# Optimization experiments

Hardware: AMD Instinct MI355X
Metric: run time of the kernel (lower is better)

## Reference

```python
import jax, jax.numpy as jnp
import numpy as np

# Model constants (match init_kwargs / torchcde conventions)
B = 1024        # batch
L = 128         # number of spline knots (grid_points = 0..L-1)
C_IN = 8        # input_channels
HID = 64        # hidden_channels
MLP_H = 128     # CDEFunc hidden width
INIT_H = 20     # initial-network hidden width


def setup_inputs() -> dict:
    key = jax.random.key(0)
    ks = jax.random.split(key, 9)
    # cubic spline coeffs: (B, L-1, 4*C_IN) laid out as [a, b, c, d] per interval
    coeffs = jax.random.normal(ks[0], (B, L - 1, 4 * C_IN), dtype=jnp.float32) * 0.1
    # initial network: C_IN -> 20 -> HID (ReLU, then Tanh)
    Wi1 = jax.random.normal(ks[1], (C_IN, INIT_H), dtype=jnp.float32) / np.sqrt(C_IN)
    bi1 = jnp.zeros((INIT_H,), jnp.float32)
    Wi2 = jax.random.normal(ks[2], (INIT_H, HID), dtype=jnp.float32) / np.sqrt(INIT_H)
    bi2 = jnp.zeros((HID,), jnp.float32)
    # CDE vector field: (HID+1) -> 128 -> C_IN*HID (ReLU, then Tanh)
    W1 = jax.random.normal(ks[3], (HID + 1, MLP_H), dtype=jnp.float32) / np.sqrt(HID + 1)
    b1 = jnp.zeros((MLP_H,), jnp.float32)
    W2 = jax.random.normal(ks[4], (MLP_H, C_IN * HID), dtype=jnp.float32) / np.sqrt(MLP_H)
    b2 = jnp.zeros((C_IN * HID,), jnp.float32)
    return {"coeffs": coeffs, "Wi1": Wi1, "bi1": bi1, "Wi2": Wi2, "bi2": bi2,
            "W1": W1, "b1": b1, "W2": W2, "b2": b2}


def reference(coeffs, Wi1, bi1, Wi2, bi2, W1, b1, W2, b2):
    Lm1 = coeffs.shape[1]
    # a,b,c,d: each (B, L-1, C_IN). X(t) = a + b*f + c*f^2 + d*f^3 on interval idx,
    # dX/dt = b + 2c*f + 3d*f^2, with f = t - idx (torchcde CubicSpline convention).
    a, b, c, d = jnp.split(coeffs, 4, axis=-1)

    def dXdt(t):
        idx = jnp.clip(jnp.floor(t).astype(jnp.int32), 0, Lm1 - 1)
        fr = t - idx
        return b[:, idx] + 2.0 * c[:, idx] * fr + 3.0 * d[:, idx] * fr * fr  # (B, C_IN)

    def cde_func(t, z):
        # FFN([HID+1, 128, C_IN*HID], ReLU hidden, Tanh output) on concat(t, z)
        tz = jnp.concatenate([jnp.full((z.shape[0], 1), t, z.dtype), z], axis=1)
        h = jax.nn.relu(tz @ W1 + b1)
        return jnp.tanh(h @ W2 + b2).reshape(z.shape[0], HID, C_IN)  # (B, HID, C_IN)

    def vf(t, z):
        # dz/dt = f(t,z) @ dX/dt
        return jnp.einsum('bhc,bc->bh', cde_func(t, z), dXdt(t))

    # z0 = initial(X(t0)); X(0) = a at interval 0 with frac 0
    X0 = a[:, 0]
    z0 = jnp.tanh(jax.nn.relu(X0 @ Wi1 + bi1) @ Wi2 + bi2)  # (B, HID)

    def rk4_step(z, i):
        t = i.astype(z.dtype)
        k1 = vf(t, z)
        k2 = vf(t + 0.5, z + 0.5 * k1)
        k3 = vf(t + 0.5, z + 0.5 * k2)
        k4 = vf(t + 1.0, z + k3)
        z_new = z + (k1 + 2.0 * k2 + 2.0 * k3 + k4) / 6.0
        return z_new, z_new

    _, zs = jax.lax.scan(rk4_step, z0, jnp.arange(Lm1))  # (L-1, B, HID)
    # z evaluated at all grid points, like cdeint(t=X.grid_points): (B, L, HID)
    return jnp.concatenate([z0[None], zs], axis=0).transpose(1, 0, 2)
```

## Files before the change

### kernel.cpp

```cpp
#include <hip/hip_runtime.h>
#include <stdint.h>

#define LM1  127
#define NTHR 512

typedef _Float16 half8_t __attribute__((ext_vector_type(8)));
typedef float    f32x4   __attribute__((ext_vector_type(4)));

__device__ __forceinline__ float fast_tanh(float x) {
  float e = __expf(2.0f * x);
  return 1.0f - 2.0f * __builtin_amdgcn_rcpf(e + 1.0f);
}

__global__ void __launch_bounds__(NTHR, 2) cde_kernel(
    const float* __restrict__ coeffs,
    const float* __restrict__ Wi1, const float* __restrict__ bi1,
    const float* __restrict__ Wi2, const float* __restrict__ bi2,
    const float* __restrict__ W1,  const float* __restrict__ b1,
    const float* __restrict__ W2,  const float* __restrict__ b2,
    float* __restrict__ out)
{
  __shared__ _Float16 zsb[16 * 72];
  __shared__ _Float16 hA [16 * 136];
  __shared__ float    fwb[8][284];
  __shared__ float    gds[2][3][4][8];

  const int t    = threadIdx.x;
  const int lane = t & 63;
  const int w    = t >> 6;
  const int l15  = lane & 15;
  const int lq   = lane >> 4;
  const int r    = lane & 3;
  const int hxl  = (lane >> 2) & 7;
  const int hx   = w * 8 + hxl;
  const int row0 = blockIdx.x * 4;
  const bool owner = (lane < 32);

  for (int u = t; u < 16 * 72 / 2;  u += NTHR) ((uint32_t*)zsb)[u] = 0u;
  for (int u = t; u < 16 * 136 / 2; u += NTHR) ((uint32_t*)hA)[u]  = 0u;

  half8_t bB[2];
  #pragma unroll
  for (int kt = 0; kt < 2; ++kt)
    #pragma unroll
    for (int j = 0; j < 8; ++j)
      bB[kt][j] = (_Float16)W1[(1 + kt * 32 + lq * 8 + j) * 128 + w * 16 + l15];
  const float w1t_c = W1[w * 16 + l15];
  const float b1_c  = b1[w * 16 + l15];

  half8_t bf[4][4];
  #pragma unroll
  for (int nt = 0; nt < 4; ++nt)
    #pragma unroll
    for (int kt = 0; kt < 4; ++kt)
      #pragma unroll
      for (int j = 0; j < 8; ++j)
        bf[nt][kt][j] =
            (_Float16)W2[(kt * 32 + lq * 8 + j) * 512 + w * 64 + nt * 16 + l15];

  float b2r[8];
  #pragma unroll
  for (int c = 0; c < 8; ++c) b2r[c] = b2[hx * 8 + c];

  float z = 0.0f;
  if (owner) {
    const float* cb = coeffs + (size_t)(row0 + r) * (LM1 * 32);
    float x0[8];
    #pragma unroll
    for (int c = 0; c < 8; ++c) x0[c] = cb[c];
    float acc = bi2[hx];
    for (int j = 0; j < 20; ++j) {
      float u = bi1[j];
      #pragma unroll
      for (int c = 0; c < 8; ++c) u += x0[c] * Wi1[c * 20 + j];
      acc += fmaxf(u, 0.0f) * Wi2[j * 64 + hx];
    }
    z = fast_tanh(acc);
    out[(size_t)(row0 + r) * 8192 + hx] = z;
  }

  const int rg = (t >> 3) & 3, cg = t & 7;
  const float* cbp = coeffs + (size_t)(row0 + rg) * (LM1 * 32);
  float pb = 0.f, pc = 0.f, pd = 0.f, pbn = 0.f;
  if (t < 32) { pb = cbp[8 + cg]; pc = cbp[16 + cg]; pd = cbp[24 + cg]; pbn = cbp[40 + cg]; }

  for (int i = 0; i < LM1; ++i) {
    if (t < 32) {
      gds[i & 1][0][rg][cg] = pb;
      gds[i & 1][1][rg][cg] = pb + pc + 0.75f * pd;
      gds[i & 1][2][rg][cg] = (i < LM1 - 1) ? pbn : fmaf(3.0f, pd, fmaf(2.0f, pc, pb));
      if (i + 1 < LM1) {
        const float* nb = cbp + (size_t)(i + 1) * 32;
        pb = nb[8 + cg]; pc = nb[16 + cg]; pd = nb[24 + cg];
        pbn = (i + 2 < LM1) ? nb[40 + cg] : 0.0f;
      }
    }

    float ksum = 0.0f, kprev = 0.0f;
    #pragma unroll
    for (int s = 0; s < 4; ++s) {
      const float coef = (s == 0) ? 0.0f : (s == 3) ? 1.0f : 0.5f;
      const float ts   = (float)i + ((s == 0) ? 0.0f : (s == 3) ? 1.0f : 0.5f);
      const int   gi   = (s == 0) ? 0 : (s == 3) ? 2 : 1;

      if (owner) zsb[r * 72 + hx] = (_Float16)(z + coef * kprev);
      __syncthreads();

      {
        half8_t a0 = *(const half8_t*)(zsb + l15 * 72 + lq * 8);
        half8_t a1 = *(const half8_t*)(zsb + l15 * 72 + 32 + lq * 8);
        f32x4 hd = {0.f, 0.f, 0.f, 0.f};
        hd = __builtin_amdgcn_mfma_f32_16x16x32_f16(a0, bB[0], hd, 0, 0, 0);
        hd = __builtin_amdgcn_mfma_f32_16x16x32_f16(a1, bB[1], hd, 0, 0, 0);
        if (lane < 16) {
          const float hb = fmaf(ts, w1t_c, b1_c);
          const int col = w * 16 + lane;
          hA[0 * 136 + col] = (_Float16)fmaxf(hd.x + hb, 0.0f);
          hA[1 * 136 + col] = (_Float16)fmaxf(hd.y + hb, 0.0f);
          hA[2 * 136 + col] = (_Float16)fmaxf(hd.z + hb, 0.0f);
          hA[3 * 136 + col] = (_Float16)fmaxf(hd.w + hb, 0.0f);
        }
      }
      __syncthreads();

      {
        half8_t ha[4];
        #pragma unroll
        for (int kt = 0; kt < 4; ++kt)
          ha[kt] = *(const half8_t*)(hA + l15 * 136 + kt * 32 + lq * 8);
        f32x4 d0 = {0.f,0.f,0.f,0.f}, d1 = d0, d2 = d0, d3 = d0;
        #pragma unroll
        for (int kt = 0; kt < 4; ++kt) {
          d0 = __builtin_amdgcn_mfma_f32_16x16x32_f16(ha[kt], bf[0][kt], d0, 0, 0, 0);
          d1 = __builtin_amdgcn_mfma_f32_16x16x32_f16(ha[kt], bf[1][kt], d1, 0, 0, 0);
          d2 = __builtin_amdgcn_mfma_f32_16x16x32_f16(ha[kt], bf[2][kt], d2, 0, 0, 0);
          d3 = __builtin_amdgcn_mfma_f32_16x16x32_f16(ha[kt], bf[3][kt], d3, 0, 0, 0);
        }
        if (lane < 16) {
          f32x4 dd[4] = {d0, d1, d2, d3};
          #pragma unroll
          for (int nt = 0; nt < 4; ++nt) {
            const int cl = nt * 16 + lane;
            *(f32x4*)(&fwb[w][36 * (cl >> 3) + 4 * (cl & 7)]) = dd[nt];
          }
        }
      }
      asm volatile("s_waitcnt lgkmcnt(0)" ::: "memory");

      if (owner) {
        const f32x4 g0 = *(const f32x4*)&gds[i & 1][gi][r][0];
        const f32x4 g1 = *(const f32x4*)&gds[i & 1][gi][r][4];
        const float gg[8] = {g0.x, g0.y, g0.z, g0.w, g1.x, g1.y, g1.z, g1.w};
        const float* fp = &fwb[w][36 * hxl + r];
        float kcv = 0.0f;
        #pragma unroll
        for (int c = 0; c < 8; ++c)
          kcv += fast_tanh(fp[4 * c] + b2r[c]) * gg[c];
        kprev = kcv;
        ksum += ((s == 1 || s == 2) ? 2.0f : 1.0f) * kcv;
      }
    }
    if (owner) {
      z += ksum * (1.0f / 6.0f);
      out[(size_t)(row0 + r) * 8192 + (size_t)(i + 1) * 64 + hx] = z;
    }
  }
}

extern "C" void kernel_launch(void* const* d_in, const int* in_sizes, int n_in,
                              void* d_out, int out_size, void* d_ws, size_t ws_size,
                              hipStream_t stream) {
  const float* coeffs = (const float*)d_in[0];
  const float* Wi1    = (const float*)d_in[1];
  const float* bi1    = (const float*)d_in[2];
  const float* Wi2    = (const float*)d_in[3];
  const float* bi2    = (const float*)d_in[4];
  const float* W1     = (const float*)d_in[5];
  const float* b1     = (const float*)d_in[6];
  const float* W2     = (const float*)d_in[7];
  const float* b2     = (const float*)d_in[8];
  float* out          = (float*)d_out;
  (void)in_sizes; (void)n_in; (void)out_size; (void)d_ws; (void)ws_size;
  cde_kernel<<<256, NTHR, 0, stream>>>(coeffs, Wi1, bi1, Wi2, bi2,
                                       W1, b1, W2, b2, out);
}
```

Measured before the change: 595.0 us.

## Split CDE vector-field work across 16 waves with swizzled LDS layouts

Doubles the block to 1024 threads so each wave computes half as many W2 output tiles (2 MFMA accumulators instead of 4). The tanh/dot epilogue is spread across all 64 lanes, with each lane handling 2 channels and combining results through xor shuffles. The z and hidden activations are stored in LDS in MFMA operand order so they can be read contiguously. The aim is to shorten the serial per-stage critical path of the RK4 loop, at the cost of more barrier participants and idle waves in the first GEMM.

```diff
diff --git a/kernel.cpp b/kernel.cpp
--- a/kernel.cpp
+++ b/kernel.cpp
@@ -2,17 +2,18 @@
 #include <stdint.h>
 
 #define LM1  127
-#define NTHR 512
+#define NTHR 1024
 
 typedef _Float16 half8_t __attribute__((ext_vector_type(8)));
 typedef float    f32x4   __attribute__((ext_vector_type(4)));
+typedef float    f32x2   __attribute__((ext_vector_type(2)));
 
 __device__ __forceinline__ float fast_tanh(float x) {
   float e = __expf(2.0f * x);
   return 1.0f - 2.0f * __builtin_amdgcn_rcpf(e + 1.0f);
 }
 
-__global__ void __launch_bounds__(NTHR, 2) cde_kernel(
+__global__ void __launch_bounds__(NTHR, 4) cde_kernel(
     const float* __restrict__ coeffs,
     const float* __restrict__ Wi1, const float* __restrict__ bi1,
     const float* __restrict__ Wi2, const float* __restrict__ bi2,
@@ -20,9 +21,9 @@
     const float* __restrict__ W2,  const float* __restrict__ b2,
     float* __restrict__ out)
 {
-  __shared__ _Float16 zsb[16 * 72];
-  __shared__ _Float16 hA [16 * 136];
-  __shared__ float    fwb[8][284];
+  __shared__ _Float16 zsb[1024];
+  __shared__ _Float16 hA [2048];
+  __shared__ float    fwb[16][144];
   __shared__ float    gds[2][3][4][8];
 
   const int t    = threadIdx.x;
@@ -31,39 +32,56 @@
   const int l15  = lane & 15;
   const int lq   = lane >> 4;
   const int r    = lane & 3;
-  const int hxl  = (lane >> 2) & 7;
-  const int hx   = w * 8 + hxl;
   const int row0 = blockIdx.x * 4;
-  const bool owner = (lane < 32);
 
-  for (int u = t; u < 16 * 72 / 2;  u += NTHR) ((uint32_t*)zsb)[u] = 0u;
-  for (int u = t; u < 16 * 136 / 2; u += NTHR) ((uint32_t*)hA)[u]  = 0u;
+  for (int u = t; u < 512;  u += NTHR) ((uint32_t*)zsb)[u] = 0u;
+  for (int u = t; u < 1024; u += NTHR) ((uint32_t*)hA)[u]  = 0u;
 
-  half8_t bB[2];
+  half8_t bB[2] = {};
+  float w1t_c = 0.f, b1_c = 0.f;
+  if (w < 8) {
+    #pragma unroll
+    for (int kt = 0; kt < 2; ++kt)
+      #pragma unroll
+      for (int j = 0; j < 8; ++j)
+        bB[kt][j] = (_Float16)W1[(1 + kt * 32 + lq * 8 + j) * 128 + w * 16 + l15];
+    w1t_c = W1[w * 16 + l15];
+    b1_c  = b1[w * 16 + l15];
+  }
+
+  half8_t bf[2][4];
   #pragma unroll
-  for (int kt = 0; kt < 2; ++kt)
-    #pragma unroll
-    for (int j = 0; j < 8; ++j)
-      bB[kt][j] = (_Float16)W1[(1 + kt * 32 + lq * 8 + j) * 128 + w * 16 + l15];
-  const float w1t_c = W1[w * 16 + l15];
-  const float b1_c  = b1[w * 16 + l15];
-
-  half8_t bf[4][4];
-  #pragma unroll
-  for (int nt = 0; nt < 4; ++nt)
+  for (int nt = 0; nt < 2; ++nt)
     #pragma unroll
     for (int kt = 0; kt < 4; ++kt)
       #pragma unroll
       for (int j = 0; j < 8; ++j)
         bf[nt][kt][j] =
-            (_Float16)W2[(kt * 32 + lq * 8 + j) * 512 + w * 64 + nt * 16 + l15];
+            (_Float16)W2[(kt * 32 + lq * 8 + j) * 512 + w * 32 + nt * 16 + l15];
 
-  float b2r[8];
-  #pragma unroll
-  for (int c = 0; c < 8; ++c) b2r[c] = b2[hx * 8 + c];
+  const int q    = lane >> 4;
+  const int hxlk = (lane >> 2) & 3;
+  const int hxk  = w * 4 + hxlk;
+  const float b2r0 = b2[hxk * 8 + 2 * q];
+  const float b2r1 = b2[hxk * 8 + 2 * q + 1];
+
+  const int hx = w * 4 + (lane >> 2);
+  _Float16* zwp;
+  {
+    const int kh = hx >> 5, lqw = (hx >> 3) & 3, j = hx & 7;
+    zwp = &zsb[8 * (kh * 64 + lqw * 16 + r) + j];
+  }
+  _Float16* hwp;
+  {
+    const int col = 16 * w + l15;
+    const int ktw = (col >> 5) & 3, lqw2 = (col >> 3) & 3, j2 = col & 7;
+    hwp = &hA[8 * (ktw * 64 + lqw2 * 16) + j2];
+  }
+  float* const fsp = &fwb[w][36 * (l15 >> 3) + 4 * (l15 & 7)];
+  const float* const frp = &fwb[w][36 * hxlk + 8 * q + r];
 
   float z = 0.0f;
-  if (owner) {
+  if (lane < 16) {
     const float* cb = coeffs + (size_t)(row0 + r) * (LM1 * 32);
     float x0[8];
     #pragma unroll
@@ -84,6 +102,8 @@
   float pb = 0.f, pc = 0.f, pd = 0.f, pbn = 0.f;
   if (t < 32) { pb = cbp[8 + cg]; pc = cbp[16 + cg]; pd = cbp[24 + cg]; pbn = cbp[40 + cg]; }
 
+  __syncthreads();
+
   for (int i = 0; i < LM1; ++i) {
     if (t < 32) {
       gds[i & 1][0][rg][cg] = pb;
@@ -103,22 +123,21 @@
       const float ts   = (float)i + ((s == 0) ? 0.0f : (s == 3) ? 1.0f : 0.5f);
       const int   gi   = (s == 0) ? 0 : (s == 3) ? 2 : 1;
 
-      if (owner) zsb[r * 72 + hx] = (_Float16)(z + coef * kprev);
+      if (lane < 16) *zwp = (_Float16)(z + coef * kprev);
       __syncthreads();
 
-      {
-        half8_t a0 = *(const half8_t*)(zsb + l15 * 72 + lq * 8);
-        half8_t a1 = *(const half8_t*)(zsb + l15 * 72 + 32 + lq * 8);
+      if (w < 8) {
+        const half8_t a0 = *(const half8_t*)(zsb + 8 * lane);
+        const half8_t a1 = *(const half8_t*)(zsb + 512 + 8 * lane);
         f32x4 hd = {0.f, 0.f, 0.f, 0.f};
         hd = __builtin_amdgcn_mfma_f32_16x16x32_f16(a0, bB[0], hd, 0, 0, 0);
         hd = __builtin_amdgcn_mfma_f32_16x16x32_f16(a1, bB[1], hd, 0, 0, 0);
         if (lane < 16) {
           const float hb = fmaf(ts, w1t_c, b1_c);
-          const int col = w * 16 + lane;
-          hA[0 * 136 + col] = (_Float16)fmaxf(hd.x + hb, 0.0f);
-          hA[1 * 136 + col] = (_Float16)fmaxf(hd.y + hb, 0.0f);
-          hA[2 * 136 + col] = (_Float16)fmaxf(hd.z + hb, 0.0f);
-          hA[3 * 136 + col] = (_Float16)fmaxf(hd.w + hb, 0.0f);
+          hwp[0]  = (_Float16)fmaxf(hd.x + hb, 0.0f);
+          hwp[8]  = (_Float16)fmaxf(hd.y + hb, 0.0f);
+          hwp[16] = (_Float16)fmaxf(hd.z + hb, 0.0f);
+          hwp[24] = (_Float16)fmaxf(hd.w + hb, 0.0f);
         }
       }
       __syncthreads();
@@ -127,40 +146,31 @@
         half8_t ha[4];
         #pragma unroll
         for (int kt = 0; kt < 4; ++kt)
-          ha[kt] = *(const half8_t*)(hA + l15 * 136 + kt * 32 + lq * 8);
-        f32x4 d0 = {0.f,0.f,0.f,0.f}, d1 = d0, d2 = d0, d3 = d0;
+          ha[kt] = *(const half8_t*)(hA + 512 * kt + 8 * lane);
+        f32x4 d0 = {0.f, 0.f, 0.f, 0.f}, d1 = d0;
         #pragma unroll
         for (int kt = 0; kt < 4; ++kt) {
           d0 = __builtin_amdgcn_mfma_f32_16x16x32_f16(ha[kt], bf[0][kt], d0, 0, 0, 0);
           d1 = __builtin_amdgcn_mfma_f32_16x16x32_f16(ha[kt], bf[1][kt], d1, 0, 0, 0);
-          d2 = __builtin_amdgcn_mfma_f32_16x16x32_f16(ha[kt], bf[2][kt], d2, 0, 0, 0);
-          d3 = __builtin_amdgcn_mfma_f32_16x16x32_f16(ha[kt], bf[3][kt], d3, 0, 0, 0);
         }
         if (lane < 16) {
-          f32x4 dd[4] = {d0, d1, d2, d3};
-          #pragma unroll
-          for (int nt = 0; nt < 4; ++nt) {
-            const int cl = nt * 16 + lane;
-            *(f32x4*)(&fwb[w][36 * (cl >> 3) + 4 * (cl & 7)]) = dd[nt];
-          }
+          *(f32x4*)(fsp)      = d0;
+          *(f32x4*)(fsp + 72) = d1;
         }
       }
       asm volatile("s_waitcnt lgkmcnt(0)" ::: "memory");
 
-      if (owner) {
-        const f32x4 g0 = *(const f32x4*)&gds[i & 1][gi][r][0];
-        const f32x4 g1 = *(const f32x4*)&gds[i & 1][gi][r][4];
-        const float gg[8] = {g0.x, g0.y, g0.z, g0.w, g1.x, g1.y, g1.z, g1.w};
-        const float* fp = &fwb[w][36 * hxl + r];
-        float kcv = 0.0f;
-        #pragma unroll
-        for (int c = 0; c < 8; ++c)
-          kcv += fast_tanh(fp[4 * c] + b2r[c]) * gg[c];
+      {
+        const float v0 = frp[0], v1 = frp[4];
+        const f32x2 gv = *(const f32x2*)&gds[i & 1][gi][r][2 * q];
+        float kcv = fast_tanh(v0 + b2r0) * gv.x + fast_tanh(v1 + b2r1) * gv.y;
+        kcv += __shfl_xor(kcv, 16, 64);
+        kcv += __shfl_xor(kcv, 32, 64);
         kprev = kcv;
         ksum += ((s == 1 || s == 2) ? 2.0f : 1.0f) * kcv;
       }
     }
-    if (owner) {
+    if (lane < 16) {
       z += ksum * (1.0f / 6.0f);
       out[(size_t)(row0 + r) * 8192 + (size_t)(i + 1) * 64 + hx] = z;
     }
```

Result: faster. 537.6 us (-9.6%).

## Split waves into dedicated layer-1 and layer-2 groups with per-wave coefficient loads

Applied to the files above, without the earlier changes.

Raises the block to 12 waves. Four waves now compute the first MLP layer, each producing 32 hidden columns, and eight waves hold W2 and compute the second layer plus the tanh and contraction. Each lane handles 4 input channels and the two halves are combined with a cross-lane shuffle. Spline coefficients are loaded as float4 directly into registers in each consumer wave, replacing the shared-memory gds staging, and the shared-memory layouts are reworked. The trade-off is a larger block and a launch bound of 3 per CU under register pressure, while the layer-1 waves sit idle during the layer-2 phase and the reverse.

```diff
diff --git a/kernel.cpp b/kernel.cpp
--- a/kernel.cpp
+++ b/kernel.cpp
@@ -2,7 +2,7 @@
 #include <stdint.h>
 
 #define LM1  127
-#define NTHR 512
+#define NTHR 768
 
 typedef _Float16 half8_t __attribute__((ext_vector_type(8)));
 typedef float    f32x4   __attribute__((ext_vector_type(4)));
@@ -12,7 +12,7 @@
   return 1.0f - 2.0f * __builtin_amdgcn_rcpf(e + 1.0f);
 }
 
-__global__ void __launch_bounds__(NTHR, 2) cde_kernel(
+__global__ void __launch_bounds__(NTHR, 3) cde_kernel(
     const float* __restrict__ coeffs,
     const float* __restrict__ Wi1, const float* __restrict__ bi1,
     const float* __restrict__ Wi2, const float* __restrict__ bi2,
@@ -20,10 +20,9 @@
     const float* __restrict__ W2,  const float* __restrict__ b2,
     float* __restrict__ out)
 {
-  __shared__ _Float16 zsb[16 * 72];
-  __shared__ _Float16 hA [16 * 136];
+  __shared__ _Float16 zsb[1024];
+  __shared__ _Float16 hA [2176];
   __shared__ float    fwb[8][284];
-  __shared__ float    gds[2][3][4][8];
 
   const int t    = threadIdx.x;
   const int lane = t & 63;
@@ -31,43 +30,60 @@
   const int l15  = lane & 15;
   const int lq   = lane >> 4;
   const int r    = lane & 3;
-  const int hxl  = (lane >> 2) & 7;
-  const int hx   = w * 8 + hxl;
   const int row0 = blockIdx.x * 4;
-  const bool owner = (lane < 32);
+  const int wc   = w - 4;
 
-  for (int u = t; u < 16 * 72 / 2;  u += NTHR) ((uint32_t*)zsb)[u] = 0u;
-  for (int u = t; u < 16 * 136 / 2; u += NTHR) ((uint32_t*)hA)[u]  = 0u;
+  for (int u = t; u < 512;  u += NTHR) ((uint32_t*)zsb)[u] = 0u;
+  for (int u = t; u < 1088; u += NTHR) ((uint32_t*)hA)[u]  = 0u;
 
-  half8_t bB[2];
-  #pragma unroll
-  for (int kt = 0; kt < 2; ++kt)
+  half8_t bB[2][2];
+  float w1t_c[2], b1_c[2];
+  if (w < 4) {
     #pragma unroll
-    for (int j = 0; j < 8; ++j)
-      bB[kt][j] = (_Float16)W1[(1 + kt * 32 + lq * 8 + j) * 128 + w * 16 + l15];
-  const float w1t_c = W1[w * 16 + l15];
-  const float b1_c  = b1[w * 16 + l15];
+    for (int nt = 0; nt < 2; ++nt) {
+      #pragma unroll
+      for (int kt = 0; kt < 2; ++kt)
+        #pragma unroll
+        for (int j = 0; j < 8; ++j)
+          bB[nt][kt][j] = (_Float16)W1[(1 + kt * 32 + lq * 8 + j) * 128 + 32 * w + nt * 16 + l15];
+      w1t_c[nt] = W1[32 * w + nt * 16 + l15];
+      b1_c[nt]  = b1[32 * w + nt * 16 + l15];
+    }
+  }
 
+  const int q  = lane >> 4;
+  const int hp = (lane >> 2) & 3;
+  const int c0 = 4 * (q >> 1);
+  const int hx = 8 * ((wc < 0) ? 0 : wc) + 4 * (q & 1) + hp;
   half8_t bf[4][4];
-  #pragma unroll
-  for (int nt = 0; nt < 4; ++nt)
+  float b2r[4];
+  f32x4 pb = {}, pc = {}, pd = {};
+  const float* grow = coeffs + (size_t)(row0 + r) * (LM1 * 32);
+  if (w >= 4) {
     #pragma unroll
-    for (int kt = 0; kt < 4; ++kt)
+    for (int nt = 0; nt < 4; ++nt)
       #pragma unroll
-      for (int j = 0; j < 8; ++j)
-        bf[nt][kt][j] =
-            (_Float16)W2[(kt * 32 + lq * 8 + j) * 512 + w * 64 + nt * 16 + l15];
+      for (int kt = 0; kt < 4; ++kt)
+        #pragma unroll
+        for (int j = 0; j < 8; ++j)
+          bf[nt][kt][j] = (_Float16)W2[(kt * 32 + lq * 8 + j) * 512 + 64 * wc + nt * 16 + l15];
+    #pragma unroll
+    for (int cc = 0; cc < 4; ++cc) b2r[cc] = b2[hx * 8 + c0 + cc];
+    pb = *(const f32x4*)(grow + 8 + c0);
+    pc = *(const f32x4*)(grow + 16 + c0);
+    pd = *(const f32x4*)(grow + 24 + c0);
+  }
 
-  float b2r[8];
-  #pragma unroll
-  for (int c = 0; c < 8; ++c) b2r[c] = b2[hx * 8 + c];
+  const bool owner = (w >= 4) && (lane < 32);
+  _Float16* const zwp = &zsb[(hx >> 5) * 512 + ((hx >> 3) & 3) * 128 + r * 8 + (hx & 7)];
+  const int ha_off = lq * 136 + l15 * 8;
+  const int kbase  = 144 * (q & 1) + 36 * hp + 16 * (q >> 1) + r;
 
   float z = 0.0f;
   if (owner) {
-    const float* cb = coeffs + (size_t)(row0 + r) * (LM1 * 32);
     float x0[8];
     #pragma unroll
-    for (int c = 0; c < 8; ++c) x0[c] = cb[c];
+    for (int c = 0; c < 8; ++c) x0[c] = grow[c - 0] ;
     float acc = bi2[hx];
     for (int j = 0; j < 20; ++j) {
       float u = bi1[j];
@@ -79,21 +95,19 @@
     out[(size_t)(row0 + r) * 8192 + hx] = z;
   }
 
-  const int rg = (t >> 3) & 3, cg = t & 7;
-  const float* cbp = coeffs + (size_t)(row0 + rg) * (LM1 * 32);
-  float pb = 0.f, pc = 0.f, pd = 0.f, pbn = 0.f;
-  if (t < 32) { pb = cbp[8 + cg]; pc = cbp[16 + cg]; pd = cbp[24 + cg]; pbn = cbp[40 + cg]; }
+  __syncthreads();
 
   for (int i = 0; i < LM1; ++i) {
-    if (t < 32) {
-      gds[i & 1][0][rg][cg] = pb;
-      gds[i & 1][1][rg][cg] = pb + pc + 0.75f * pd;
-      gds[i & 1][2][rg][cg] = (i < LM1 - 1) ? pbn : fmaf(3.0f, pd, fmaf(2.0f, pc, pb));
-      if (i + 1 < LM1) {
-        const float* nb = cbp + (size_t)(i + 1) * 32;
-        pb = nb[8 + cg]; pc = nb[16 + cg]; pd = nb[24 + cg];
-        pbn = (i + 2 < LM1) ? nb[40 + cg] : 0.0f;
-      }
+    f32x4 g0 = {}, g1 = {}, g2 = {};
+    if (w >= 4) {
+      g0 = pb;
+      g1 = pb + pc + 0.75f * pd;
+      const f32x4 glast = pb + 2.0f * pc + 3.0f * pd;
+      const float* np = grow + (size_t)((i + 1 < LM1) ? i + 1 : LM1 - 1) * 32;
+      pb = *(const f32x4*)(np + 8 + c0);
+      pc = *(const f32x4*)(np + 16 + c0);
+      pd = *(const f32x4*)(np + 24 + c0);
+      g2 = (i < LM1 - 1) ? pb : glast;
     }
 
     float ksum = 0.0f, kprev = 0.0f;
@@ -101,34 +115,36 @@
     for (int s = 0; s < 4; ++s) {
       const float coef = (s == 0) ? 0.0f : (s == 3) ? 1.0f : 0.5f;
       const float ts   = (float)i + ((s == 0) ? 0.0f : (s == 3) ? 1.0f : 0.5f);
-      const int   gi   = (s == 0) ? 0 : (s == 3) ? 2 : 1;
 
-      if (owner) zsb[r * 72 + hx] = (_Float16)(z + coef * kprev);
+      if (owner) *zwp = (_Float16)(z + coef * kprev);
       __syncthreads();
 
-      {
-        half8_t a0 = *(const half8_t*)(zsb + l15 * 72 + lq * 8);
-        half8_t a1 = *(const half8_t*)(zsb + l15 * 72 + 32 + lq * 8);
-        f32x4 hd = {0.f, 0.f, 0.f, 0.f};
-        hd = __builtin_amdgcn_mfma_f32_16x16x32_f16(a0, bB[0], hd, 0, 0, 0);
-        hd = __builtin_amdgcn_mfma_f32_16x16x32_f16(a1, bB[1], hd, 0, 0, 0);
-        if (lane < 16) {
-          const float hb = fmaf(ts, w1t_c, b1_c);
-          const int col = w * 16 + lane;
-          hA[0 * 136 + col] = (_Float16)fmaxf(hd.x + hb, 0.0f);
-          hA[1 * 136 + col] = (_Float16)fmaxf(hd.y + hb, 0.0f);
-          hA[2 * 136 + col] = (_Float16)fmaxf(hd.z + hb, 0.0f);
-          hA[3 * 136 + col] = (_Float16)fmaxf(hd.w + hb, 0.0f);
+      if (w < 4) {
+        const half8_t a0 = *(const half8_t*)(zsb + 8 * lane);
+        const half8_t a1 = *(const half8_t*)(zsb + 512 + 8 * lane);
+        #pragma unroll
+        for (int nt = 0; nt < 2; ++nt) {
+          f32x4 hd = {0.f, 0.f, 0.f, 0.f};
+          hd = __builtin_amdgcn_mfma_f32_16x16x32_f16(a0, bB[nt][0], hd, 0, 0, 0);
+          hd = __builtin_amdgcn_mfma_f32_16x16x32_f16(a1, bB[nt][1], hd, 0, 0, 0);
+          if (lane < 16) {
+            const float hb = fmaf(ts, w1t_c[nt], b1_c[nt]);
+            _Float16* hw = &hA[w * 544 + (2 * nt + (l15 >> 3)) * 136 + (l15 & 7)];
+            hw[0]  = (_Float16)fmaxf(hd.x + hb, 0.0f);
+            hw[8]  = (_Float16)fmaxf(hd.y + hb, 0.0f);
+            hw[16] = (_Float16)fmaxf(hd.z + hb, 0.0f);
+            hw[24] = (_Float16)fmaxf(hd.w + hb, 0.0f);
+          }
         }
       }
       __syncthreads();
 
-      {
+      if (w >= 4) {
         half8_t ha[4];
         #pragma unroll
         for (int kt = 0; kt < 4; ++kt)
-          ha[kt] = *(const half8_t*)(hA + l15 * 136 + kt * 32 + lq * 8);
-        f32x4 d0 = {0.f,0.f,0.f,0.f}, d1 = d0, d2 = d0, d3 = d0;
+          ha[kt] = *(const half8_t*)(hA + kt * 544 + ha_off);
+        f32x4 d0 = {0.f, 0.f, 0.f, 0.f}, d1 = d0, d2 = d0, d3 = d0;
         #pragma unroll
         for (int kt = 0; kt < 4; ++kt) {
           d0 = __builtin_amdgcn_mfma_f32_16x16x32_f16(ha[kt], bf[0][kt], d0, 0, 0, 0);
@@ -139,23 +155,18 @@
         if (lane < 16) {
           f32x4 dd[4] = {d0, d1, d2, d3};
           #pragma unroll
-          for (int nt = 0; nt < 4; ++nt) {
-            const int cl = nt * 16 + lane;
-            *(f32x4*)(&fwb[w][36 * (cl >> 3) + 4 * (cl & 7)]) = dd[nt];
-          }
+          for (int nt = 0; nt < 4; ++nt)
+            *(f32x4*)(&fwb[wc][72 * nt + 4 * l15 + 4 * (l15 >> 3)]) = dd[nt];
         }
-      }
-      asm volatile("s_waitcnt lgkmcnt(0)" ::: "memory");
+        asm volatile("s_waitcnt lgkmcnt(0)" ::: "memory");
 
-      if (owner) {
-        const f32x4 g0 = *(const f32x4*)&gds[i & 1][gi][r][0];
-        const f32x4 g1 = *(const f32x4*)&gds[i & 1][gi][r][4];
-        const float gg[8] = {g0.x, g0.y, g0.z, g0.w, g1.x, g1.y, g1.z, g1.w};
-        const float* fp = &fwb[w][36 * hxl + r];
-        float kcv = 0.0f;
-        #pragma unroll
-        for (int c = 0; c < 8; ++c)
-          kcv += fast_tanh(fp[4 * c] + b2r[c]) * gg[c];
+        const f32x4 gg = (s == 0) ? g0 : (s == 3) ? g2 : g1;
+        const float* fp = &fwb[wc][kbase];
+        float kcv = fast_tanh(fp[0]  + b2r[0]) * gg.x
+                  + fast_tanh(fp[4]  + b2r[1]) * gg.y
+                  + fast_tanh(fp[8]  + b2r[2]) * gg.z
+                  + fast_tanh(fp[12] + b2r[3]) * gg.w;
+        kcv += __shfl_xor(kcv, 32, 64);
         kprev = kcv;
         ksum += ((s == 1 || s == 2) ? 2.0f : 1.0f) * kcv;
       }
```

Result: slower. 675.8 us (+13.6%).
